# Kernel optimization log

Measured on AMD Instinct MI355X. Metric: run time of the kernel, lower is better.

The kernel has to match this reference:

```python
import jax, jax.numpy as jnp
import numpy as np

NH = 50000; NO = 50000; E = 500000; D = 256; L = 8; B = 512; C = 117


def setup_inputs() -> dict:
    key = jax.random.key(0)
    ks = jax.random.split(key, 32)
    s = 0.05
    inp = {
        'x_human': jax.random.normal(ks[0], (NH, D), jnp.float32),
        'x_object': jax.random.normal(ks[1], (NO, D), jnp.float32),
        'edge_index_ho': jax.random.randint(ks[2], (2, E), 0, NH),
        'edge_index_oh': jax.random.randint(ks[3], (2, E), 0, NO),
        'edge_attr_ho': jax.random.normal(ks[4], (E, 2), jnp.float32),
        'edge_attr_oh': jax.random.normal(ks[5], (E, 2), jnp.float32),
        'hbatch': jnp.sort(jax.random.randint(ks[6], (NH,), 0, B)),
        'obatch': jnp.sort(jax.random.randint(ks[7], (NO,), 0, B)),
    }
    # GATConv params per relation, stacked over L layers
    names = ['Wsrc', 'Wdst', 'asrc', 'adst', 'Wedge', 'aedge', 'bias']
    shapes = [(L, D, D), (L, D, D), (L, D), (L, D), (L, 2, D), (L, D), (L, D)]
    i = 8
    for rel in ['ho', 'oh']:
        for n, sh in zip(names, shapes):
            inp[f'{n}_{rel}'] = jax.random.normal(ks[i], sh, jnp.float32) * s
            i += 1
    inp['W_emlp'] = jax.random.normal(ks[i], (2, 32), jnp.float32) * s
    inp['b_emlp'] = jnp.zeros((32,), jnp.float32)
    inp['W_p1'] = jax.random.normal(ks[i + 1], (2 * D + 32, C), jnp.float32) * s
    inp['b_p1'] = jnp.zeros((C,), jnp.float32)
    inp['W_p2'] = jax.random.normal(ks[i + 2], (2 * D + 32, C), jnp.float32) * s
    inp['b_p2'] = jnp.zeros((C,), jnp.float32)
    return inp


def _gat(x_src, x_dst, ei, ea, Wsrc, Wdst, asrc, adst, Wedge, aedge, bias, num_dst):
    # PyG GATConv (heads=1, edge_dim=2, add_self_loops=False)
    h_src = x_src @ Wsrc                       # [Ns, D]
    h_dst = x_dst @ Wdst                       # [Nd, D]
    src, dst = ei[0], ei[1]
    a_s = h_src @ asrc                         # [Ns]
    a_d = h_dst @ adst                         # [Nd]
    a_e = (ea @ Wedge) @ aedge                 # [E]
    logit = jax.nn.leaky_relu(a_s[src] + a_d[dst] + a_e, 0.2)
    m = jax.ops.segment_max(logit, dst, num_segments=num_dst)
    ex = jnp.exp(logit - m[dst])
    denom = jax.ops.segment_sum(ex, dst, num_segments=num_dst)
    alpha = ex / denom[dst]                    # segment softmax over dst
    out = jax.ops.segment_sum(h_src[src] * alpha[:, None], dst, num_segments=num_dst)
    return out + bias


def _seg_mean(x, seg, num):
    s = jax.ops.segment_sum(x, seg, num_segments=num)
    cnt = jax.ops.segment_sum(jnp.ones((x.shape[0],), x.dtype), seg, num_segments=num)
    return s / jnp.maximum(cnt, 1.0)[:, None]


def reference(x_human, x_object, edge_index_ho, edge_index_oh, edge_attr_ho,
              edge_attr_oh, hbatch, obatch,
              Wsrc_ho, Wdst_ho, asrc_ho, adst_ho, Wedge_ho, aedge_ho, bias_ho,
              Wsrc_oh, Wdst_oh, asrc_oh, adst_oh, Wedge_oh, aedge_oh, bias_oh,
              W_emlp, b_emlp, W_p1, b_p1, W_p2, b_p2):
    xh, xo = x_human, x_object
    ph, po = None, None
    for l in range(L):
        nxo = _gat(xh, xo, edge_index_ho, edge_attr_ho, Wsrc_ho[l], Wdst_ho[l],
                   asrc_ho[l], adst_ho[l], Wedge_ho[l], aedge_ho[l], bias_ho[l], NO)
        nxh = _gat(xo, xh, edge_index_oh, edge_attr_oh, Wsrc_oh[l], Wdst_oh[l],
                   asrc_oh[l], adst_oh[l], Wedge_oh[l], aedge_oh[l], bias_oh[l], NH)
        nxh = jax.nn.relu(nxh)
        nxo = jax.nn.relu(nxo)
        if ph is not None:
            nxh = nxh + ph
            nxo = nxo + po
        ph, po = nxh, nxo
        xh, xo = nxh, nxo
    hpool = _seg_mean(xh, hbatch, B)           # [B, D]
    opool = _seg_mean(xo, obatch, B)           # [B, D]
    ea = jax.nn.relu(edge_attr_ho @ W_emlp + b_emlp)  # [E, 32]
    edge_batch = hbatch[edge_index_ho[0]]
    epool = _seg_mean(ea, edge_batch, B)       # [B, 32]
    graph_emb = jnp.concatenate([hpool, opool, epool], axis=-1)  # [B, 544]
    l1 = jax.nn.softmax(graph_emb @ W_p1 + b_p1, axis=1)
    l2 = jax.nn.softmax(graph_emb @ W_p2 + b_p2, axis=1)
    return jnp.stack((l1, l2), axis=1)         # [B, 2, C]
```

## Files before the change

kernel.cpp:

```cpp
#include <hip/hip_runtime.h>
#include <math.h>


#define NNODE 50000
#define EDG   500000
#define DIM   256
#define LAY   8
#define BB    512
#define CC    117
#define EMBD  544
#define SCB   49
#define HW    16384
#define HC    16
#define HNW   4

typedef short bf16x8 __attribute__((ext_vector_type(8)));
typedef float f32x4  __attribute__((ext_vector_type(4)));

static __device__ __forceinline__ float lrelu(float x){ return x >= 0.f ? x : 0.2f*x; }
static __device__ __forceinline__ unsigned short f2b(float f){
  unsigned int u = __float_as_uint(f);
  unsigned int r = (u + 0x7fffu + ((u >> 16) & 1u)) >> 16;
  return (unsigned short)r;
}
static __device__ __forceinline__ float b2f(unsigned short u){
  return __uint_as_float(((unsigned int)u) << 16);
}

__global__ void vcompute_k(const float* __restrict__ Wsho, const float* __restrict__ Wdho,
                           const float* __restrict__ asho, const float* __restrict__ adho,
                           const float* __restrict__ Wsoh, const float* __restrict__ Wdoh,
                           const float* __restrict__ asoh, const float* __restrict__ adoh,
                           float* __restrict__ vbuf){
  int gid = blockIdx.x*blockDim.x + threadIdx.x;
  int wv = gid >> 6, lane = gid & 63;
  if (wv >= 32*DIM) return;
  int p = wv >> 8, k = wv & 255;
  int which = p & 1, rel = (p>>1)&1, l = p>>2;
  const float* W; const float* a;
  if (rel==0){ W = which? Wdho : Wsho; a = which? adho : asho; }
  else       { W = which? Wdoh : Wsoh; a = which? adoh : asoh; }
  W += (size_t)l*DIM*DIM; a += (size_t)l*DIM;
  const float4* w4 = (const float4*)(W + (size_t)k*DIM);
  const float4* a4 = (const float4*)a;
  float4 wv4 = w4[lane], av4 = a4[lane];
  float s = wv4.x*av4.x + wv4.y*av4.y + wv4.z*av4.z + wv4.w*av4.w;
  for (int off=32; off; off>>=1) s += __shfl_xor(s, off);
  if (lane==0) vbuf[(size_t)p*DIM + k] = s;
}

__global__ void wecompute_k(const float* __restrict__ Weho, const float* __restrict__ aeho,
                            const float* __restrict__ Weoh, const float* __restrict__ aeoh,
                            float* __restrict__ webuf){
  int blk = blockIdx.x;
  int rel = blk & 1, l = blk >> 1;
  const float* We = rel? Weoh : Weho;
  const float* ae = rel? aeoh : aeho;
  int lane = threadIdx.x;
  const float4* w0 = (const float4*)(We + (size_t)l*2*DIM);
  const float4* w1 = (const float4*)(We + (size_t)l*2*DIM + DIM);
  const float4* a4 = (const float4*)(ae + (size_t)l*DIM);
  float4 av = a4[lane], x0 = w0[lane], x1 = w1[lane];
  float s0 = x0.x*av.x + x0.y*av.y + x0.z*av.z + x0.w*av.w;
  float s1 = x1.x*av.x + x1.y*av.y + x1.z*av.z + x1.w*av.w;
  for (int off=32; off; off>>=1){ s0 += __shfl_xor(s0, off); s1 += __shfl_xor(s1, off); }
  if (lane==0){ webuf[blk*2] = s0; webuf[blk*2+1] = s1; }
}

__global__ void histp_k(const int* __restrict__ ei_ho, const int* __restrict__ ei_oh,
                        int* __restrict__ phist){
  __shared__ int h[HW];
  int x = blockIdx.x, y = blockIdx.y, z = blockIdx.z, t = threadIdx.x;
  for (int i=t; i<HW; i+=256) h[i] = 0;
  __syncthreads();
  const int* keys = (z==0)? (ei_ho + EDG) : (z==1)? (ei_oh + EDG) : ei_ho;
  int lo = y << 14;
  int e0 = x * (EDG/HC), e1 = e0 + (EDG/HC);
  for (int e = e0 + t; e < e1; e += 256){
    int k = keys[e] - lo;
    if ((unsigned)k < (unsigned)HW) atomicAdd(&h[k], 1);
  }
  __syncthreads();
  int* dst = phist + (size_t)(((z*HNW + y)*HC + x))*HW;
  for (int i=t; i<HW; i+=256) dst[i] = h[i];
}

static __device__ __forceinline__ int4 phist_sum4(const int* __restrict__ phist,
                                                  int z, int idx){
  int win = idx >> 14, off = idx & (HW-1);
  const int* base = phist + (size_t)((z*HNW + win)*HC)*HW + off;
  int4 s = make_int4(0,0,0,0);
  #pragma unroll
  for (int c=0;c<HC;c++){
    int4 v = *(const int4*)(base + (size_t)c*HW);
    s.x += v.x; s.y += v.y; s.z += v.z; s.w += v.w;
  }
  return s;
}

__global__ void scanA_k(const int* __restrict__ phist, int* __restrict__ bsum){
  __shared__ int sh[256];
  int y = blockIdx.y, b = blockIdx.x, t = threadIdx.x;
  int idx = b*1024 + t*4;
  int s = 0;
  if (idx + 3 < NNODE){
    int4 v = phist_sum4(phist, y, idx);
    s = v.x + v.y + v.z + v.w;
  } else {
    for (int j=0;j<4;j++) if (idx+j < NNODE){
      int win = (idx+j) >> 14, off = (idx+j) & (HW-1);
      for (int c=0;c<HC;c++) s += phist[(size_t)((y*HNW+win)*HC+c)*HW + off];
    }
  }
  sh[t] = s; __syncthreads();
  for (int off=128; off; off>>=1){ if (t<off) sh[t] += sh[t+off]; __syncthreads(); }
  if (t==0) bsum[y*SCB + b] = sh[0];
}

__global__ void scanB_k(int* __restrict__ bsum, int* __restrict__ boff,
                        int* __restrict__ rp0, int* __restrict__ rp1, int* __restrict__ rp2){
  int t = threadIdx.x;
  if (t >= 3) return;
  int run = 0;
  for (int i=0;i<SCB;i++){ boff[t*SCB+i] = run; run += bsum[t*SCB+i]; }
  int* rp = (t==0)? rp0 : (t==1)? rp1 : rp2;
  rp[NNODE] = run;
}

__global__ void scanC_k(const int* __restrict__ phist, const int* __restrict__ boff,
                        int* __restrict__ rp0, int* __restrict__ rp1, int* __restrict__ rp2){
  __shared__ int sh[256];
  int y = blockIdx.y, b = blockIdx.x, t = threadIdx.x;
  int* rp = (y==0)? rp0 : (y==1)? rp1 : rp2;
  int idx = b*1024 + t*4;
  int c[4] = {0,0,0,0};
  if (idx + 3 < NNODE){
    int4 v = phist_sum4(phist, y, idx);
    c[0]=v.x; c[1]=v.y; c[2]=v.z; c[3]=v.w;
  } else {
    for (int j=0;j<4;j++) if (idx+j < NNODE){
      int win = (idx+j) >> 14, off = (idx+j) & (HW-1);
      for (int cc=0;cc<HC;cc++) c[j] += phist[(size_t)((y*HNW+win)*HC+cc)*HW + off];
    }
  }
  int mysum = c[0]+c[1]+c[2]+c[3];
  sh[t] = mysum; __syncthreads();
  for (int off=1; off<256; off<<=1){
    int v = (t>=off) ? sh[t-off] : 0;
    __syncthreads();
    sh[t] += v;
    __syncthreads();
  }
  int base = boff[y*SCB + b] + (sh[t] - mysum);
  int run = 0;
  for (int j=0;j<4;j++){
    if (idx+j < NNODE) rp[idx+j] = base + run;
    run += c[j];
  }
}

__global__ void scatter3_k(const int* __restrict__ ei_ho, const int* __restrict__ ei_oh,
                           const float* __restrict__ ea_ho, const float* __restrict__ ea_oh,
                           const int* __restrict__ rp0, const int* __restrict__ rp1,
                           const int* __restrict__ rp2, int* __restrict__ cur,
                           int* __restrict__ srcs0, int* __restrict__ srcs1,
                           float2* __restrict__ eap0, float2* __restrict__ eap1,
                           float2* __restrict__ eap2){
  int e = blockIdx.x*blockDim.x + threadIdx.x;
  if (e >= EDG) return;
  int y = blockIdx.y;
  if (y == 0){
    int d = ei_ho[EDG + e];
    int pos = rp0[d] + atomicAdd(&cur[d], 1);
    srcs0[pos] = ei_ho[e];
    eap0[pos] = make_float2(ea_ho[2*e], ea_ho[2*e+1]);
  } else if (y == 1){
    int d = ei_oh[EDG + e];
    int pos = rp1[d] + atomicAdd(&cur[NNODE + d], 1);
    srcs1[pos] = ei_oh[e];
    eap1[pos] = make_float2(ea_oh[2*e], ea_oh[2*e+1]);
  } else {
    int s = ei_ho[e];
    int pos = rp2[s] + atomicAdd(&cur[2*NNODE + s], 1);
    eap2[pos] = make_float2(ea_ho[2*e], ea_ho[2*e+1]);
  }
}

__global__ void xcdg_k(const float* __restrict__ xh_in, const float* __restrict__ xo_in,
                       unsigned short* __restrict__ xhb, unsigned short* __restrict__ xob,
                       const float* __restrict__ vbuf, float* __restrict__ aset){
  int gid = blockIdx.x*blockDim.x + threadIdx.x;
  int w = gid >> 6, lane = gid & 63;
  if (w >= NNODE) return;
  int z = blockIdx.y;
  const float* X = z? xo_in : xh_in;
  unsigned short* O = z? xob : xhb;
  const float* v1 = vbuf + (size_t)(z? 2:0)*DIM;
  const float* v2 = vbuf + (size_t)(z? 1:3)*DIM;
  float* o1 = aset + (size_t)(z? 2:0)*NNODE;
  float* o2 = aset + (size_t)(z? 1:3)*NNODE;
  float4 xv = ((const float4*)(X + (size_t)w*DIM))[lane];
  ushort4 ob; ob.x=f2b(xv.x); ob.y=f2b(xv.y); ob.z=f2b(xv.z); ob.w=f2b(xv.w);
  ((ushort4*)O)[(size_t)w*64 + lane] = ob;
  float4 a = ((const float4*)v1)[lane];
  float4 b = ((const float4*)v2)[lane];
  float s1 = xv.x*a.x + xv.y*a.y + xv.z*a.z + xv.w*a.w;
  float s2 = xv.x*b.x + xv.y*b.y + xv.z*b.z + xv.w*b.w;
  for (int off=32; off; off>>=1){ s1 += __shfl_xor(s1, off); s2 += __shfl_xor(s2, off); }
  if (lane==0){ o1[w] = s1; o2[w] = s2; }
}

__global__ void wtconv_k(const float* __restrict__ Who, const float* __restrict__ Woh,
                         unsigned short* __restrict__ Wt){
  int gid = blockIdx.x*blockDim.x + threadIdx.x;
  int rel = gid >> 19;
  int rem = gid & ((1<<19)-1);
  int l = rem >> 16;
  int idx = rem & 65535;
  int n = idx >> 8, k = idx & 255;
  const float* W = rel ? Woh : Who;
  Wt[gid] = f2b(W[(size_t)l*65536 + (size_t)k*256 + n]);
}

__global__ __launch_bounds__(256) void gemmb2_k(const unsigned short* __restrict__ A0,
                                                const unsigned short* __restrict__ A1,
                                                const unsigned short* __restrict__ B0,
                                                const unsigned short* __restrict__ B1,
                                                unsigned short* __restrict__ H0,
                                                unsigned short* __restrict__ H1, int M){
  __shared__ __align__(16) unsigned short As[4096];
  __shared__ __align__(16) unsigned short Bs[4096];
  int z = blockIdx.z;
  const unsigned short* A  = z? A1 : A0;
  const unsigned short* Bt = z? B1 : B0;
  unsigned short* H        = z? H1 : H0;
  int tid = threadIdx.x;
  int col0 = blockIdx.x * 128;
  int row0 = blockIdx.y * 128;
  int w = tid >> 6, lane = tid & 63;
  int q = lane >> 4, ml = lane & 15;
  f32x4 acc[2][8];
  #pragma unroll
  for (int i=0;i<2;i++)
    #pragma unroll
    for (int j=0;j<8;j++) acc[i][j] = (f32x4){0.f,0.f,0.f,0.f};
  int srow = tid >> 2;
  int sq   = tid & 3;
  for (int k0 = 0; k0 < 256; k0 += 32){
    #pragma unroll
    for (int p = 0; p < 2; ++p){
      int row = p*64 + srow;
      int gr = row0 + row;
      uint4 av = make_uint4(0,0,0,0);
      if (gr < M) av = *(const uint4*)(A + (size_t)gr*256 + k0 + sq*8);
      *(uint4*)&As[((((row>>4)*4) + sq)*16 + (row&15))*8] = av;
      int gc = col0 + row;
      uint4 bv = *(const uint4*)(Bt + (size_t)gc*256 + k0 + sq*8);
      *(uint4*)&Bs[((((row>>4)*4) + sq)*16 + (row&15))*8] = bv;
    }
    __syncthreads();
    bf16x8 a0 = *(const bf16x8*)&As[(((2*w+0)*4 + q)*16 + ml)*8];
    bf16x8 a1 = *(const bf16x8*)&As[(((2*w+1)*4 + q)*16 + ml)*8];
    #pragma unroll
    for (int nf = 0; nf < 8; ++nf){
      bf16x8 b = *(const bf16x8*)&Bs[((nf*4 + q)*16 + ml)*8];
      acc[0][nf] = __builtin_amdgcn_mfma_f32_16x16x32_bf16(a0, b, acc[0][nf], 0,0,0);
      acc[1][nf] = __builtin_amdgcn_mfma_f32_16x16x32_bf16(a1, b, acc[1][nf], 0,0,0);
    }
    __syncthreads();
  }
  #pragma unroll
  for (int mf = 0; mf < 2; ++mf){
    #pragma unroll
    for (int r = 0; r < 4; ++r){
      int gr = row0 + 32*w + 16*mf + q*4 + r;
      if (gr < M){
        #pragma unroll
        for (int nf = 0; nf < 8; ++nf)
          H[(size_t)gr*256 + col0 + nf*16 + ml] = f2b(acc[mf][nf][r]);
      }
    }
  }
}

__global__ void attn2_k(const int* __restrict__ rp0, const int* __restrict__ srcs0,
                        const float2* __restrict__ eap0,
                        const int* __restrict__ rp1, const int* __restrict__ srcs1,
                        const float2* __restrict__ eap1,
                        const float* __restrict__ cur_a, float* __restrict__ nxt_a,
                        const float* __restrict__ wepl,
                        const unsigned short* __restrict__ hs0,
                        const unsigned short* __restrict__ hs1,
                        const float* __restrict__ bias0, const float* __restrict__ bias1,
                        const unsigned short* __restrict__ xprev0,
                        const unsigned short* __restrict__ xprev1,
                        unsigned short* __restrict__ xnext0,
                        unsigned short* __restrict__ xnext1,
                        const float* __restrict__ vbl,
                        int hasRes, int doNext){
  int gid = blockIdx.x*blockDim.x + threadIdx.x;
  int w = gid >> 6, lane = gid & 63;
  if (w >= NNODE) return;
  int rel = blockIdx.y;
  const int* rowptr = rel? rp1 : rp0;
  const int* srcs   = rel? srcs1 : srcs0;
  const float2* eaperm = rel? eap1 : eap0;
  const float* a_s = cur_a + (size_t)(rel? 2:0)*NNODE;
  const float* a_d = cur_a + (size_t)(rel? 3:1)*NNODE;
  float w0 = wepl[rel? 2:0], w1 = wepl[rel? 3:1];
  const unsigned short* hs = rel? hs1 : hs0;
  const float* bias = rel? bias1 : bias0;
  const unsigned short* xprev = rel? xprev1 : xprev0;
  unsigned short* xnext = rel? xnext1 : xnext0;

  int st = rowptr[w], en = rowptr[w+1];
  int deg = en - st;
  float adv = a_d[w];
  float ax=0.f, ay=0.f, az=0.f, aw=0.f;
  const ushort4* h4 = (const ushort4*)hs;
  if (deg > 0 && deg <= 64){
    int sreg = 0; float lg = -INFINITY;
    if (lane < deg){
      sreg = srcs[st + lane];
      float2 ev = eaperm[st + lane];
      lg = lrelu(a_s[sreg] + adv + ev.x*w0 + ev.y*w1);
    }
    float mx = lg;
    for (int off=32; off; off>>=1) mx = fmaxf(mx, __shfl_xor(mx, off));
    float ex = (lane < deg) ? expf(lg - mx) : 0.f;
    float sm = ex;
    for (int off=32; off; off>>=1) sm += __shfl_xor(sm, off);
    float wgt = ex / sm;
    int i = 0;
    for (; i + 7 < deg; i += 8){
      float wi[8]; int si[8];
      #pragma unroll
      for (int j=0;j<8;j++){ wi[j] = __shfl(wgt, i+j); si[j] = __shfl(sreg, i+j); }
      ushort4 hv[8];
      #pragma unroll
      for (int j=0;j<8;j++) hv[j] = h4[(size_t)si[j]*64 + lane];
      #pragma unroll
      for (int j=0;j<8;j++){
        ax += wi[j]*b2f(hv[j].x); ay += wi[j]*b2f(hv[j].y);
        az += wi[j]*b2f(hv[j].z); aw += wi[j]*b2f(hv[j].w);
      }
    }
    for (; i + 3 < deg; i += 4){
      float wi[4]; int si[4];
      #pragma unroll
      for (int j=0;j<4;j++){ wi[j] = __shfl(wgt, i+j); si[j] = __shfl(sreg, i+j); }
      ushort4 hv[4];
      #pragma unroll
      for (int j=0;j<4;j++) hv[j] = h4[(size_t)si[j]*64 + lane];
      #pragma unroll
      for (int j=0;j<4;j++){
        ax += wi[j]*b2f(hv[j].x); ay += wi[j]*b2f(hv[j].y);
        az += wi[j]*b2f(hv[j].z); aw += wi[j]*b2f(hv[j].w);
      }
    }
    for (; i < deg; ++i){
      float wi = __shfl(wgt, i);
      int   si = __shfl(sreg, i);
      ushort4 hv = h4[(size_t)si*64 + lane];
      ax += wi*b2f(hv.x); ay += wi*b2f(hv.y); az += wi*b2f(hv.z); aw += wi*b2f(hv.w);
    }
  } else if (deg > 64){
    float mx = -INFINITY;
    for (int p = st + lane; p < en; p += 64){
      float2 ev = eaperm[p];
      float lg = lrelu(a_s[srcs[p]] + adv + ev.x*w0 + ev.y*w1);
      mx = fmaxf(mx, lg);
    }
    for (int off=32; off; off>>=1) mx = fmaxf(mx, __shfl_xor(mx, off));
    float sm = 0.f;
    for (int p = st + lane; p < en; p += 64){
      float2 ev = eaperm[p];
      float lg = lrelu(a_s[srcs[p]] + adv + ev.x*w0 + ev.y*w1);
      sm += expf(lg - mx);
    }
    for (int off=32; off; off>>=1) sm += __shfl_xor(sm, off);
    float inv = 1.f/sm;
    for (int p = st; p < en; ++p){
      float2 ev = eaperm[p];
      int s = srcs[p];
      float lg = lrelu(a_s[s] + adv + ev.x*w0 + ev.y*w1);
      float wgt = expf(lg - mx) * inv;
      ushort4 hv = h4[(size_t)s*64 + lane];
      ax += wgt*b2f(hv.x); ay += wgt*b2f(hv.y); az += wgt*b2f(hv.z); aw += wgt*b2f(hv.w);
    }
  }
  float4 bv = ((const float4*)bias)[lane];
  float4 o;
  o.x = fmaxf(ax + bv.x, 0.f);
  o.y = fmaxf(ay + bv.y, 0.f);
  o.z = fmaxf(az + bv.z, 0.f);
  o.w = fmaxf(aw + bv.w, 0.f);
  if (hasRes){
    ushort4 r = ((const ushort4*)xprev)[(size_t)w*64 + lane];
    o.x += b2f(r.x); o.y += b2f(r.y); o.z += b2f(r.z); o.w += b2f(r.w);
  }
  ushort4 ob; ob.x=f2b(o.x); ob.y=f2b(o.y); ob.z=f2b(o.z); ob.w=f2b(o.w);
  ((ushort4*)xnext)[(size_t)w*64 + lane] = ob;
  if (doNext){
    const float* vsn = vbl + (size_t)(rel? 0:2)*DIM;
    const float* vdn = vbl + (size_t)(rel? 3:1)*DIM;
    float* asn = nxt_a + (size_t)(rel? 0:2)*NNODE;
    float* adn = nxt_a + (size_t)(rel? 3:1)*NNODE;
    float4 a = ((const float4*)vsn)[lane];
    float4 b = ((const float4*)vdn)[lane];
    float s1 = o.x*a.x + o.y*a.y + o.z*a.z + o.w*a.w;
    float s2 = o.x*b.x + o.y*b.y + o.z*b.z + o.w*b.w;
    for (int off=32; off; off>>=1){ s1 += __shfl_xor(s1, off); s2 += __shfl_xor(s2, off); }
    if (lane==0){ asn[w] = s1; adn[w] = s2; }
  }
}

__device__ __forceinline__ int lowerb(const int* a, int n, int v){
  int lo=0, hi=n;
  while (lo < hi){ int m = (lo+hi)>>1; if (a[m] < v) lo = m+1; else hi = m; }
  return lo;
}

__global__ void pool2_k(const unsigned short* __restrict__ xh, const unsigned short* __restrict__ xo,
                        const int* __restrict__ hbatch, const int* __restrict__ obatch,
                        float* __restrict__ hpool, float* __restrict__ opool){
  int z = blockIdx.y;
  const unsigned short* x = z? xo : xh;
  const int* batch = z? obatch : hbatch;
  float* out = z? opool : hpool;
  int b = blockIdx.x, t = threadIdx.x;
  int st = lowerb(batch, NNODE, b), en = lowerb(batch, NNODE, b+1);
  float s = 0.f;
  for (int i=st;i<en;i++) s += b2f(x[(size_t)i*DIM + t]);
  out[(size_t)b*DIM + t] = s / fmaxf((float)(en - st), 1.f);
}

__global__ void epool_k(const int* __restrict__ rp_src, const int* __restrict__ hbatch,
                        const float2* __restrict__ eaperm, const float* __restrict__ Wem,
                        const float* __restrict__ bem, float* __restrict__ epool){
  __shared__ float ps[8][33];
  int b = blockIdx.x, t = threadIdx.x;
  int j = t & 31, g = t >> 5;
  int nst = lowerb(hbatch, NNODE, b), nen = lowerb(hbatch, NNODE, b+1);
  int est = rp_src[nst], een = rp_src[nen];
  float w0 = Wem[j], w1 = Wem[32+j], bb = bem[j];
  float s = 0.f;
  for (int p = est + g; p < een; p += 8){
    float2 e = eaperm[p];
    s += fmaxf(e.x*w0 + e.y*w1 + bb, 0.f);
  }
  ps[g][j] = s; __syncthreads();
  if (g == 0){
    float tot = 0.f;
    #pragma unroll
    for (int gg=0; gg<8; gg++) tot += ps[gg][j];
    epool[(size_t)b*32 + j] = tot / fmaxf((float)(een - est), 1.f);
  }
}

__global__ void head_k(const float* __restrict__ hpool, const float* __restrict__ opool,
                       const float* __restrict__ epool,
                       const float* __restrict__ Wp1, const float* __restrict__ bp1,
                       const float* __restrict__ Wp2, const float* __restrict__ bp2,
                       float* __restrict__ out){
  __shared__ float emb[EMBD];
  __shared__ float red[256];
  int b = blockIdx.x, t = threadIdx.x;
  emb[t] = hpool[(size_t)b*DIM + t];
  emb[DIM + t] = opool[(size_t)b*DIM + t];
  if (t < 32) emb[2*DIM + t] = epool[(size_t)b*32 + t];
  __syncthreads();
  for (int h = 0; h < 2; ++h){
    const float* Wp = h? Wp2 : Wp1;
    const float* bp = h? bp2 : bp1;
    float logit = -INFINITY;
    if (t < CC){
      float s = bp[t];
      for (int k=0;k<EMBD;k++) s += emb[k]*Wp[(size_t)k*CC + t];
      logit = s;
    }
    red[t] = logit; __syncthreads();
    for (int off=128; off; off>>=1){ if (t<off) red[t] = fmaxf(red[t], red[t+off]); __syncthreads(); }
    float mx = red[0]; __syncthreads();
    float ex = (t < CC) ? expf(logit - mx) : 0.f;
    red[t] = ex; __syncthreads();
    for (int off=128; off; off>>=1){ if (t<off) red[t] += red[t+off]; __syncthreads(); }
    float sm = red[0]; __syncthreads();
    if (t < CC) out[((size_t)b*2 + h)*CC + t] = ex / sm;
  }
}

extern "C" void kernel_launch(void* const* d_in, const int* in_sizes, int n_in,
                              void* d_out, int out_size, void* d_ws, size_t ws_size,
                              hipStream_t stream) {
  (void)in_sizes; (void)n_in; (void)out_size; (void)ws_size;
  const float* xh_in   = (const float*)d_in[0];
  const float* xo_in   = (const float*)d_in[1];
  const int*   ei_ho   = (const int*)d_in[2];
  const int*   ei_oh   = (const int*)d_in[3];
  const float* ea_ho   = (const float*)d_in[4];
  const float* ea_oh   = (const float*)d_in[5];
  const int*   hbatch  = (const int*)d_in[6];
  const int*   obatch  = (const int*)d_in[7];
  const float* Wsrc_ho = (const float*)d_in[8];
  const float* Wdst_ho = (const float*)d_in[9];
  const float* asrc_ho = (const float*)d_in[10];
  const float* adst_ho = (const float*)d_in[11];
  const float* Wedge_ho= (const float*)d_in[12];
  const float* aedge_ho= (const float*)d_in[13];
  const float* bias_ho = (const float*)d_in[14];
  const float* Wsrc_oh = (const float*)d_in[15];
  const float* Wdst_oh = (const float*)d_in[16];
  const float* asrc_oh = (const float*)d_in[17];
  const float* adst_oh = (const float*)d_in[18];
  const float* Wedge_oh= (const float*)d_in[19];
  const float* aedge_oh= (const float*)d_in[20];
  const float* bias_oh = (const float*)d_in[21];
  const float* W_emlp  = (const float*)d_in[22];
  const float* b_emlp  = (const float*)d_in[23];
  const float* W_p1    = (const float*)d_in[24];
  const float* b_p1    = (const float*)d_in[25];
  const float* W_p2    = (const float*)d_in[26];
  const float* b_p2    = (const float*)d_in[27];
  float* out = (float*)d_out;

  size_t ND = (size_t)NNODE*DIM;
  float* f = (float*)d_ws;
  float* aset0 = f;
  float* aset1 = aset0 + 4*NNODE;
  float* vbuf  = aset1 + 4*NNODE;
  float* webuf = vbuf + 32*DIM;
  float* hpool = webuf + 32;
  float* opool = hpool + (size_t)BB*DIM;
  float* epool = opool + (size_t)BB*DIM;
  float2* eap_ho  = (float2*)(epool + (size_t)BB*32);
  float2* eap_oh  = eap_ho + EDG;
  float2* eap_src = eap_oh + EDG;
  unsigned short* xhb0 = (unsigned short*)(eap_src + EDG);
  unsigned short* xhb1 = xhb0 + ND;
  unsigned short* xob0 = xhb1 + ND;
  unsigned short* xob1 = xob0 + ND;
  unsigned short* hSb0 = xob1 + ND;
  unsigned short* hSb1 = hSb0 + ND;
  unsigned short* Wtb  = hSb1 + ND;
  int* cur     = (int*)(Wtb + (size_t)2*LAY*DIM*DIM);
  int* rp_ho   = cur + 3*NNODE;
  int* rp_oh   = rp_ho + NNODE + 1;
  int* rp_src  = rp_oh + NNODE + 1;
  int* srcs_ho = rp_src + NNODE + 1;
  int* srcs_oh = srcs_ho + EDG;
  int* bsum    = srcs_oh + EDG;
  int* boff    = bsum + 3*SCB;
  int* phist   = boff + 3*SCB;

  hipMemsetAsync(cur, 0, sizeof(int)*3*NNODE, stream);
  vcompute_k<<<2048, 256, 0, stream>>>(Wsrc_ho, Wdst_ho, asrc_ho, adst_ho,
                                       Wsrc_oh, Wdst_oh, asrc_oh, adst_oh, vbuf);
  wecompute_k<<<16, 64, 0, stream>>>(Wedge_ho, aedge_ho, Wedge_oh, aedge_oh, webuf);
  wtconv_k<<<4096, 256, 0, stream>>>(Wsrc_ho, Wsrc_oh, Wtb);
  histp_k<<<dim3(HC, HNW, 3), 256, 0, stream>>>(ei_ho, ei_oh, phist);
  scanA_k<<<dim3(SCB, 3), 256, 0, stream>>>(phist, bsum);
  scanB_k<<<1, 64, 0, stream>>>(bsum, boff, rp_ho, rp_oh, rp_src);
  scanC_k<<<dim3(SCB, 3), 256, 0, stream>>>(phist, boff, rp_ho, rp_oh, rp_src);
  scatter3_k<<<dim3(1954, 3), 256, 0, stream>>>(ei_ho, ei_oh, ea_ho, ea_oh,
                                                rp_ho, rp_oh, rp_src, cur,
                                                srcs_ho, srcs_oh, eap_ho, eap_oh, eap_src);
  xcdg_k<<<dim3(12500, 2), 256, 0, stream>>>(xh_in, xo_in, xhb1, xob1, vbuf, aset0);

  const unsigned short* xh = xhb1;
  const unsigned short* xo = xob1;
  unsigned short* xh_bufs[2] = {xhb0, xhb1};
  unsigned short* xo_bufs[2] = {xob0, xob1};
  float* asets[2] = {aset0, aset1};
  for (int l = 0; l < LAY; ++l){
    unsigned short* xo_n = xo_bufs[l & 1];
    unsigned short* xh_n = xh_bufs[l & 1];
    float* cur_a = asets[l & 1];
    float* nxt_a = asets[(l & 1) ^ 1];
    int doNext = (l < LAY-1);
    int ln = doNext ? (l+1) : l;
    gemmb2_k<<<dim3(2, 391, 2), 256, 0, stream>>>(xh, xo,
                                                  Wtb + (size_t)l*DIM*DIM,
                                                  Wtb + (size_t)(LAY + l)*DIM*DIM,
                                                  hSb0, hSb1, NNODE);
    attn2_k<<<dim3(12500, 2), 256, 0, stream>>>(rp_ho, srcs_ho, eap_ho,
                                                rp_oh, srcs_oh, eap_oh,
                                                cur_a, nxt_a,
                                                webuf + (size_t)l*4,
                                                hSb0, hSb1,
                                                bias_ho + (size_t)l*DIM, bias_oh + (size_t)l*DIM,
                                                xo, xh, xo_n, xh_n,
                                                vbuf + (size_t)ln*4*DIM,
                                                l > 0, doNext);
    xh = xh_n; xo = xo_n;
  }

  pool2_k<<<dim3(BB, 2), 256, 0, stream>>>(xh, xo, hbatch, obatch, hpool, opool);
  epool_k<<<BB, 256, 0, stream>>>(rp_src, hbatch, eap_src, W_emlp, b_emlp, epool);
  head_k<<<BB, 256, 0, stream>>>(hpool, opool, epool, W_p1, b_p1, W_p2, b_p2, out);
}
```

Before: 1.553 ms.

## Pack edge records into float4 and use direct global-to-LDS loads in GEMM

Edge source indices and the two edge attributes are packed into one 16-byte record per CSR slot, so the attention kernel issues a single vector load per edge instead of two separate loads. Separately, the bf16 GEMM tile staging is changed to use global_load_lds, copying global memory straight into LDS without passing through registers. Rows past M are clamped to the last row rather than zero-filled. The record packing adds an unused padding float, which raises edge-metadata bandwidth.

```diff
diff --git a/kernel.cpp b/kernel.cpp
--- a/kernel.cpp
+++ b/kernel.cpp
@@ -25,6 +25,12 @@
 }
 static __device__ __forceinline__ float b2f(unsigned short u){
   return __uint_as_float(((unsigned int)u) << 16);
+}
+
+static __device__ __forceinline__ void gload_lds16(const void* g, void* l){
+  __builtin_amdgcn_global_load_lds((const __attribute__((address_space(1))) void*)g,
+                                   (__attribute__((address_space(3))) void*)l,
+                                   16, 0, 0);
 }
 
 __global__ void vcompute_k(const float* __restrict__ Wsho, const float* __restrict__ Wdho,
@@ -163,8 +169,7 @@
                            const float* __restrict__ ea_ho, const float* __restrict__ ea_oh,
                            const int* __restrict__ rp0, const int* __restrict__ rp1,
                            const int* __restrict__ rp2, int* __restrict__ cur,
-                           int* __restrict__ srcs0, int* __restrict__ srcs1,
-                           float2* __restrict__ eap0, float2* __restrict__ eap1,
+                           float4* __restrict__ rec0, float4* __restrict__ rec1,
                            float2* __restrict__ eap2){
   int e = blockIdx.x*blockDim.x + threadIdx.x;
   if (e >= EDG) return;
@@ -172,13 +177,11 @@
   if (y == 0){
     int d = ei_ho[EDG + e];
     int pos = rp0[d] + atomicAdd(&cur[d], 1);
-    srcs0[pos] = ei_ho[e];
-    eap0[pos] = make_float2(ea_ho[2*e], ea_ho[2*e+1]);
+    rec0[pos] = make_float4(__int_as_float(ei_ho[e]), ea_ho[2*e], ea_ho[2*e+1], 0.f);
   } else if (y == 1){
     int d = ei_oh[EDG + e];
     int pos = rp1[d] + atomicAdd(&cur[NNODE + d], 1);
-    srcs1[pos] = ei_oh[e];
-    eap1[pos] = make_float2(ea_oh[2*e], ea_oh[2*e+1]);
+    rec1[pos] = make_float4(__int_as_float(ei_oh[e]), ea_oh[2*e], ea_oh[2*e+1], 0.f);
   } else {
     int s = ei_ho[e];
     int pos = rp2[s] + atomicAdd(&cur[2*NNODE + s], 1);
@@ -244,19 +247,25 @@
   for (int i=0;i<2;i++)
     #pragma unroll
     for (int j=0;j<8;j++) acc[i][j] = (f32x4){0.f,0.f,0.f,0.f};
-  int srow = tid >> 2;
-  int sq   = tid & 3;
+
+  const unsigned short* srcA[2];
+  const unsigned short* srcB[2];
+  #pragma unroll
+  for (int p=0;p<2;p++){
+    int c = p*256 + w*64 + lane;
+    int row = ((c>>6)<<4) | (c&15);
+    int sq  = (c>>4)&3;
+    int gr = row0 + row; if (gr >= M) gr = M-1;
+    srcA[p] = A  + (size_t)gr*256 + sq*8;
+    srcB[p] = Bt + (size_t)(col0 + row)*256 + sq*8;
+  }
+
   for (int k0 = 0; k0 < 256; k0 += 32){
     #pragma unroll
     for (int p = 0; p < 2; ++p){
-      int row = p*64 + srow;
-      int gr = row0 + row;
-      uint4 av = make_uint4(0,0,0,0);
-      if (gr < M) av = *(const uint4*)(A + (size_t)gr*256 + k0 + sq*8);
-      *(uint4*)&As[((((row>>4)*4) + sq)*16 + (row&15))*8] = av;
-      int gc = col0 + row;
-      uint4 bv = *(const uint4*)(Bt + (size_t)gc*256 + k0 + sq*8);
-      *(uint4*)&Bs[((((row>>4)*4) + sq)*16 + (row&15))*8] = bv;
+      gload_lds16(srcA[p], &As[(size_t)(p*256 + w*64)*8]);
+      gload_lds16(srcB[p], &Bs[(size_t)(p*256 + w*64)*8]);
+      srcA[p] += 32; srcB[p] += 32;
     }
     __syncthreads();
     bf16x8 a0 = *(const bf16x8*)&As[(((2*w+0)*4 + q)*16 + ml)*8];
@@ -283,10 +292,8 @@
   }
 }
 
-__global__ void attn2_k(const int* __restrict__ rp0, const int* __restrict__ srcs0,
-                        const float2* __restrict__ eap0,
-                        const int* __restrict__ rp1, const int* __restrict__ srcs1,
-                        const float2* __restrict__ eap1,
+__global__ void attn2_k(const int* __restrict__ rp0, const float4* __restrict__ rec0,
+                        const int* __restrict__ rp1, const float4* __restrict__ rec1,
                         const float* __restrict__ cur_a, float* __restrict__ nxt_a,
                         const float* __restrict__ wepl,
                         const unsigned short* __restrict__ hs0,
@@ -303,8 +310,7 @@
   if (w >= NNODE) return;
   int rel = blockIdx.y;
   const int* rowptr = rel? rp1 : rp0;
-  const int* srcs   = rel? srcs1 : srcs0;
-  const float2* eaperm = rel? eap1 : eap0;
+  const float4* rec = rel? rec1 : rec0;
   const float* a_s = cur_a + (size_t)(rel? 2:0)*NNODE;
   const float* a_d = cur_a + (size_t)(rel? 3:1)*NNODE;
   float w0 = wepl[rel? 2:0], w1 = wepl[rel? 3:1];
@@ -321,9 +327,9 @@
   if (deg > 0 && deg <= 64){
     int sreg = 0; float lg = -INFINITY;
     if (lane < deg){
-      sreg = srcs[st + lane];
-      float2 ev = eaperm[st + lane];
-      lg = lrelu(a_s[sreg] + adv + ev.x*w0 + ev.y*w1);
+      float4 r = rec[st + lane];
+      sreg = __float_as_int(r.x);
+      lg = lrelu(a_s[sreg] + adv + r.y*w0 + r.z*w1);
     }
     float mx = lg;
     for (int off=32; off; off>>=1) mx = fmaxf(mx, __shfl_xor(mx, off));
@@ -367,23 +373,23 @@
   } else if (deg > 64){
     float mx = -INFINITY;
     for (int p = st + lane; p < en; p += 64){
-      float2 ev = eaperm[p];
-      float lg = lrelu(a_s[srcs[p]] + adv + ev.x*w0 + ev.y*w1);
+      float4 r = rec[p];
+      float lg = lrelu(a_s[__float_as_int(r.x)] + adv + r.y*w0 + r.z*w1);
       mx = fmaxf(mx, lg);
     }
     for (int off=32; off; off>>=1) mx = fmaxf(mx, __shfl_xor(mx, off));
     float sm = 0.f;
     for (int p = st + lane; p < en; p += 64){
-      float2 ev = eaperm[p];
-      float lg = lrelu(a_s[srcs[p]] + adv + ev.x*w0 + ev.y*w1);
+      float4 r = rec[p];
+      float lg = lrelu(a_s[__float_as_int(r.x)] + adv + r.y*w0 + r.z*w1);
       sm += expf(lg - mx);
     }
     for (int off=32; off; off>>=1) sm += __shfl_xor(sm, off);
     float inv = 1.f/sm;
     for (int p = st; p < en; ++p){
-      float2 ev = eaperm[p];
-      int s = srcs[p];
-      float lg = lrelu(a_s[s] + adv + ev.x*w0 + ev.y*w1);
+      float4 r = rec[p];
+      int s = __float_as_int(r.x);
+      float lg = lrelu(a_s[s] + adv + r.y*w0 + r.z*w1);
       float wgt = expf(lg - mx) * inv;
       ushort4 hv = h4[(size_t)s*64 + lane];
       ax += wgt*b2f(hv.x); ay += wgt*b2f(hv.y); az += wgt*b2f(hv.z); aw += wgt*b2f(hv.w);
@@ -533,9 +539,9 @@
   float* hpool = webuf + 32;
   float* opool = hpool + (size_t)BB*DIM;
   float* epool = opool + (size_t)BB*DIM;
-  float2* eap_ho  = (float2*)(epool + (size_t)BB*32);
-  float2* eap_oh  = eap_ho + EDG;
-  float2* eap_src = eap_oh + EDG;
+  float4* rec_ho  = (float4*)(epool + (size_t)BB*32);
+  float4* rec_oh  = rec_ho + EDG;
+  float2* eap_src = (float2*)(rec_oh + EDG);
   unsigned short* xhb0 = (unsigned short*)(eap_src + EDG);
   unsigned short* xhb1 = xhb0 + ND;
   unsigned short* xob0 = xhb1 + ND;
@@ -547,9 +553,7 @@
   int* rp_ho   = cur + 3*NNODE;
   int* rp_oh   = rp_ho + NNODE + 1;
   int* rp_src  = rp_oh + NNODE + 1;
-  int* srcs_ho = rp_src + NNODE + 1;
-  int* srcs_oh = srcs_ho + EDG;
-  int* bsum    = srcs_oh + EDG;
+  int* bsum    = rp_src + NNODE + 1;
   int* boff    = bsum + 3*SCB;
   int* phist   = boff + 3*SCB;
 
@@ -564,7 +568,7 @@
   scanC_k<<<dim3(SCB, 3), 256, 0, stream>>>(phist, boff, rp_ho, rp_oh, rp_src);
   scatter3_k<<<dim3(1954, 3), 256, 0, stream>>>(ei_ho, ei_oh, ea_ho, ea_oh,
                                                 rp_ho, rp_oh, rp_src, cur,
-                                                srcs_ho, srcs_oh, eap_ho, eap_oh, eap_src);
+                                                rec_ho, rec_oh, eap_src);
   xcdg_k<<<dim3(12500, 2), 256, 0, stream>>>(xh_in, xo_in, xhb1, xob1, vbuf, aset0);
 
   const unsigned short* xh = xhb1;
@@ -583,8 +587,8 @@
                                                   Wtb + (size_t)l*DIM*DIM,
                                                   Wtb + (size_t)(LAY + l)*DIM*DIM,
                                                   hSb0, hSb1, NNODE);
-    attn2_k<<<dim3(12500, 2), 256, 0, stream>>>(rp_ho, srcs_ho, eap_ho,
-                                                rp_oh, srcs_oh, eap_oh,
+    attn2_k<<<dim3(12500, 2), 256, 0, stream>>>(rp_ho, rec_ho,
+                                                rp_oh, rec_oh,
                                                 cur_a, nxt_a,
                                                 webuf + (size_t)l*4,
                                                 hSb0, hSb1,
```

After: 1.503 ms. -3.2%, faster.
